# Performance work log

Measured on AMD Instinct MI355X. Metric: run time of the kernel, lower is better.

Reference implementation:

```python
import jax, jax.numpy as jnp
import numpy as np
import math

B, T, C = 4, 2048, 2048
NUM_HEADS = 16
HEAD_DIM = C // NUM_HEADS  # 128
ROPE_BASE = 10000.0


def _rope_tables(t, head_dim, dtype):
    # inv_freq over even dims; emb = concat(freqs, freqs)
    inv_freq = 1.0 / (ROPE_BASE ** (jnp.arange(0, head_dim, 2, dtype=jnp.float32) / head_dim))
    pos = jnp.arange(t, dtype=jnp.float32)
    freqs = jnp.einsum('i,j->ij', pos, inv_freq)          # [t, head_dim/2]
    emb = jnp.concatenate([freqs, freqs], axis=-1)        # [t, head_dim]
    return jnp.cos(emb).astype(dtype), jnp.sin(emb).astype(dtype)


def _rotate_half(x):
    x1, x2 = jnp.split(x, 2, axis=-1)
    return jnp.concatenate([-x2, x1], axis=-1)


def setup_inputs() -> dict:
    key = jax.random.key(0)
    ks = jax.random.split(key, 5)
    scale = 1.0 / math.sqrt(C)
    x = jax.random.normal(ks[0], (B, T, C), dtype=jnp.float32)
    wq = jax.random.normal(ks[1], (C, C), dtype=jnp.float32) * scale
    wk = jax.random.normal(ks[2], (C, C), dtype=jnp.float32) * scale
    wv = jax.random.normal(ks[3], (C, C), dtype=jnp.float32) * scale
    wo = jax.random.normal(ks[4], (C, C), dtype=jnp.float32) * scale
    mask = jnp.tril(jnp.ones((T, T), dtype=jnp.int32))[None, None]  # causal [1,1,T,T]
    return {"x": x, "mask": mask, "wq": wq, "wk": wk, "wv": wv, "wo": wo}


def reference(x, mask, wq, wk, wv, wo):
    b, t, c = x.shape
    h, hd = NUM_HEADS, HEAD_DIM
    # torch Linear: y = x @ W.T (W is [out,in])
    q = (x @ wq.T).reshape(b, t, h, hd).transpose(0, 2, 1, 3)  # [b,h,t,hd]
    k = (x @ wk.T).reshape(b, t, h, hd).transpose(0, 2, 1, 3)
    v = (x @ wv.T).reshape(b, t, h, hd).transpose(0, 2, 1, 3)
    cos, sin = _rope_tables(t, hd, x.dtype)  # [t,hd] each, broadcast over b,h
    q = q * cos + _rotate_half(q) * sin
    k = k * cos + _rotate_half(k) * sin
    att = jnp.einsum('bhqd,bhkd->bhqk', q, k) * (1.0 / math.sqrt(hd))
    att = jnp.where(mask == 0, -jnp.inf, att)
    att = jax.nn.softmax(att, axis=-1)
    y = jnp.einsum('bhqk,bhkd->bhqd', att, v)
    y = y.transpose(0, 2, 1, 3).reshape(b, t, c)
    return y @ wo.T
```

## Files before the change

### kernel.cpp

```cpp
#include <hip/hip_runtime.h>
#include <hip/hip_bf16.h>

#define BB 4
#define TT 2048
#define CC 2048
#define NH 16
#define HD 128
#define BT (BB*TT)

using u16 = unsigned short;
typedef __bf16 bf16x8 __attribute__((ext_vector_type(8)));
typedef float  f32x4  __attribute__((ext_vector_type(4)));

#define AS1 __attribute__((address_space(1)))
#define AS3 __attribute__((address_space(3)))

__device__ __forceinline__ float b2f(u16 u){ return __uint_as_float(((unsigned)u) << 16); }
__device__ __forceinline__ u16 f2b(float f){
  unsigned u = __float_as_uint(f);
  u += 0x7FFFu + ((u >> 16) & 1u);
  return (u16)(u >> 16);
}
__device__ __forceinline__ void gld_lds16(const u16* g, u16* l){
  __builtin_amdgcn_global_load_lds((const AS1 void*)g, (AS3 void*)l, 16, 0, 0);
}

__global__ __launch_bounds__(256) void cvt_kernel(const float* __restrict__ in,
                                                  u16* __restrict__ out, int n8)
{
  const int i = blockIdx.x * 256 + threadIdx.x;
  if (i >= n8) return;
  const float4 a = ((const float4*)in)[2*i];
  const float4 b = ((const float4*)in)[2*i + 1];
  uint4 pk;
  pk.x = (unsigned)f2b(a.x) | ((unsigned)f2b(a.y) << 16);
  pk.y = (unsigned)f2b(a.z) | ((unsigned)f2b(a.w) << 16);
  pk.z = (unsigned)f2b(b.x) | ((unsigned)f2b(b.y) << 16);
  pk.w = (unsigned)f2b(b.z) | ((unsigned)f2b(b.w) << 16);
  ((uint4*)out)[i] = pk;
}

template<bool OUT_BF16>
__global__ __launch_bounds__(512, 2) void gemm256(const u16* __restrict__ A,
                                                  const u16* __restrict__ W,
                                                  void* __restrict__ Cv,
                                                  int K, int N,
                                                  long wz, long cz)
{
  __shared__ u16 lds[65536];
  const int tid  = threadIdx.x;
  const int lane = tid & 63;
  const int wid  = tid >> 6;
  const int wm   = wid >> 2;
  const int wn   = wid & 3;

  const u16* Wz = W + (size_t)blockIdx.z * wz;

  const int nwg  = (int)(gridDim.x * gridDim.y);
  const int orig = (int)(blockIdx.y * gridDim.x + blockIdx.x);
  const int swz  = (orig & 7) * (nwg >> 3) + (orig >> 3);
  const int bx   = swz % (int)gridDim.x;
  const int by   = swz / (int)gridDim.x;
  const long mbase = (long)by * 256;
  const long nbase = (long)bx * 256;

  const int sR  = tid >> 2;
  const int sG8 = (((tid & 3) ^ (sR & 3)) << 3);
  const u16* gA = A  + (mbase + sR) * (long)K + sG8;
  const u16* gB = Wz + (nbase + sR) * (long)K + sG8;
  const long rowK = (long)128 * K;

  const int n   = lane & 15;
  const int g   = lane >> 4;
  const int sl8 = ((g ^ (n & 3)) << 3);
  const int aoff = (wm*128 + n)*32 + sl8;
  const int boff = 8192 + (wn*64 + n)*32 + sl8;

  f32x4 acc[8][4] = {};
  const int NT = K >> 5;

#define STAGE_A(bufi, tt) do { \
    u16* d_ = lds + (bufi)*16384 + tid*8; \
    gld_lds16(gA + (long)(tt)*32,        d_); \
    gld_lds16(gA + rowK + (long)(tt)*32, d_ + 4096); } while(0)
#define STAGE_B(bufi, tt) do { \
    u16* d_ = lds + (bufi)*16384 + 8192 + tid*8; \
    gld_lds16(gB + (long)(tt)*32,        d_); \
    gld_lds16(gB + rowK + (long)(tt)*32, d_ + 4096); } while(0)

  STAGE_A(0, 0); STAGE_B(0, 0);
  STAGE_A(1, 1); STAGE_B(1, 1);
  STAGE_A(2, 2); STAGE_B(2, 2);
  asm volatile("s_waitcnt vmcnt(4)" ::: "memory");
  __builtin_amdgcn_s_barrier();
  asm volatile("" ::: "memory");

  bf16x8 pa0A[4], pb0A[4], a1A[4], pa0B[4], pb0B[4], a1B[4];
  #pragma unroll
  for (int i = 0; i < 4; i++) pa0A[i] = *(const bf16x8*)&lds[aoff + i*512];
  #pragma unroll
  for (int j = 0; j < 4; j++) pb0A[j] = *(const bf16x8*)&lds[boff + j*512];

  for (int t = 0; t < NT; t += 2) {
    {
      const u16* Ab = lds + (t & 3) * 16384;
      const u16* Nb = lds + ((t+1) & 3) * 16384;
      if (t + 3 < NT) STAGE_A((t+3)&3, t+3);
      #pragma unroll
      for (int i = 0; i < 4; i++) a1A[i]  = *(const bf16x8*)&Ab[aoff + (i+4)*512];
      #pragma unroll
      for (int i = 0; i < 4; i++) pa0B[i] = *(const bf16x8*)&Nb[aoff + i*512];
      #pragma unroll
      for (int j = 0; j < 4; j++) pb0B[j] = *(const bf16x8*)&Nb[boff + j*512];
      if (t + 3 < NT) STAGE_B((t+3)&3, t+3);
      __builtin_amdgcn_s_setprio(1);
      #pragma unroll
      for (int i = 0; i < 4; i++)
        #pragma unroll
        for (int j = 0; j < 4; j++)
          acc[i][j] = __builtin_amdgcn_mfma_f32_16x16x32_bf16(pa0A[i], pb0A[j], acc[i][j], 0,0,0);
      #pragma unroll
      for (int i = 0; i < 4; i++)
        #pragma unroll
        for (int j = 0; j < 4; j++)
          acc[i+4][j] = __builtin_amdgcn_mfma_f32_16x16x32_bf16(a1A[i], pb0A[j], acc[i+4][j], 0,0,0);
      __builtin_amdgcn_s_setprio(0);
      if (t + 3 < NT) { asm volatile("s_waitcnt vmcnt(4)" ::: "memory"); }
      else            { asm volatile("s_waitcnt vmcnt(0)" ::: "memory"); }
      __builtin_amdgcn_s_barrier();
      asm volatile("" ::: "memory");
    }
    {
      const int u = t + 1;
      const u16* Ab = lds + (u & 3) * 16384;
      if (u + 3 < NT) STAGE_A((u+3)&3, u+3);
      #pragma unroll
      for (int i = 0; i < 4; i++) a1B[i] = *(const bf16x8*)&Ab[aoff + (i+4)*512];
      if (u + 1 < NT) {
        const u16* Nb = lds + ((u+1) & 3) * 16384;
        #pragma unroll
        for (int i = 0; i < 4; i++) pa0A[i] = *(const bf16x8*)&Nb[aoff + i*512];
        #pragma unroll
        for (int j = 0; j < 4; j++) pb0A[j] = *(const bf16x8*)&Nb[boff + j*512];
      }
      if (u + 3 < NT) STAGE_B((u+3)&3, u+3);
      __builtin_amdgcn_s_setprio(1);
      #pragma unroll
      for (int i = 0; i < 4; i++)
        #pragma unroll
        for (int j = 0; j < 4; j++)
          acc[i][j] = __builtin_amdgcn_mfma_f32_16x16x32_bf16(pa0B[i], pb0B[j], acc[i][j], 0,0,0);
      #pragma unroll
      for (int i = 0; i < 4; i++)
        #pragma unroll
        for (int j = 0; j < 4; j++)
          acc[i+4][j] = __builtin_amdgcn_mfma_f32_16x16x32_bf16(a1B[i], pb0B[j], acc[i+4][j], 0,0,0);
      __builtin_amdgcn_s_setprio(0);
      if (u + 3 < NT) { asm volatile("s_waitcnt vmcnt(4)" ::: "memory"); }
      else            { asm volatile("s_waitcnt vmcnt(0)" ::: "memory"); }
      __builtin_amdgcn_s_barrier();
      asm volatile("" ::: "memory");
    }
  }
#undef STAGE_A
#undef STAGE_B

  const int crow0 = g * 4;
  u16*   C16 = (u16*)Cv   + (size_t)blockIdx.z * cz;
  float* C32 = (float*)Cv;
  #pragma unroll
  for (int i = 0; i < 8; i++)
    #pragma unroll
    for (int j = 0; j < 4; j++)
      #pragma unroll
      for (int r = 0; r < 4; r++) {
        const long row = mbase + wm*128 + i*16 + crow0 + r;
        const long col = nbase + wn*64  + j*16 + n;
        if (OUT_BF16) C16[row*N + col] = f2b(acc[i][j][r]);
        else          C32[row*N + col] = acc[i][j][r];
      }
}

__global__ __launch_bounds__(256) void rope_kernel(u16* __restrict__ q, u16* __restrict__ k)
{
  const unsigned idx = blockIdx.x * 256u + threadIdx.x;
  const int d = idx & 63;
  const int h = (idx >> 6) & 15;
  const int t = (idx >> 10) & 2047;
  const int b = idx >> 21;
  const float inv = __expf(-9.210340371976184f * ((float)d * (1.0f/64.0f)));
  const float ang = (float)t * inv;
  float sn, cs;
  sincosf(ang, &sn, &cs);
  const size_t base = ((size_t)(b * TT + t)) * CC + (size_t)h * HD + d;
  const float q0 = b2f(q[base]), q1 = b2f(q[base + 64]);
  q[base]      = f2b(q0*cs - q1*sn);
  q[base + 64] = f2b(q1*cs + q0*sn);
  const float k0 = b2f(k[base]), k1 = b2f(k[base + 64]);
  k[base]      = f2b(k0*cs - k1*sn);
  k[base + 64] = f2b(k1*cs + k0*sn);
}

__global__ __launch_bounds__(256) void transpose_v(const u16* __restrict__ v,
                                                   u16* __restrict__ vt)
{
  __shared__ u16 L[64][136];
  const int tid = threadIdx.x;
  const int t0 = blockIdx.x * 64;
  const int b = blockIdx.y >> 4, h = blockIdx.y & 15;
  #pragma unroll
  for (int it = 0; it < 4; it++) {
    const int row = (tid >> 4) + it*16;
    const int c8 = (tid & 15) * 8;
    *(uint4*)&L[row][c8] = *(const uint4*)(v + ((size_t)(b*TT + t0 + row))*CC + h*HD + c8);
  }
  __syncthreads();
  #pragma unroll
  for (int it = 0; it < 4; it++) {
    const int hd = (tid >> 3) + it*32;
    const int c = (tid & 7) * 8;
    u16 tmp[8];
    #pragma unroll
    for (int j = 0; j < 8; j++) tmp[j] = L[c + j][hd];
    uint4 pk;
    pk.x = (unsigned)tmp[0] | ((unsigned)tmp[1] << 16);
    pk.y = (unsigned)tmp[2] | ((unsigned)tmp[3] << 16);
    pk.z = (unsigned)tmp[4] | ((unsigned)tmp[5] << 16);
    pk.w = (unsigned)tmp[6] | ((unsigned)tmp[7] << 16);
    *(uint4*)(vt + ((size_t)((b*NH + h)*HD + hd))*TT + t0 + c) = pk;
  }
}

#define PS_ST 72
#define OB_ST 136
__global__ __launch_bounds__(256, 2) void attn_mfma(const u16* __restrict__ q,
                                                    const u16* __restrict__ k,
                                                    const u16* __restrict__ vt,
                                                    u16* __restrict__ y)
{
  __shared__ u16 smem[2*64*128 + 128*64 + 4*32*PS_ST];
  u16* Ks = smem;
  u16* Vs = smem + 16384;
  u16* Ps = smem + 16384 + 8192;

  const int tid  = threadIdx.x;
  const int lane = tid & 63;
  const int w    = tid >> 6;
  const int n    = lane & 15;
  const int g    = lane >> 4;
  const int k8   = g * 8;
  const int nx   = n & 7;
  const int qb   = (int)gridDim.x - 1 - (int)blockIdx.x;
  const int bh   = blockIdx.y;
  const int b = bh >> 4, h = bh & 15;

  const u16* Qg  = q  + (size_t)b*TT*CC + (size_t)h*HD;
  const u16* Kg  = k  + (size_t)b*TT*CC + (size_t)h*HD;
  const u16* Vtg = vt + ((size_t)(b*NH + h)*HD) * TT;
  u16*       Yg  = y  + (size_t)b*TT*CC + (size_t)h*HD;

  const int ksrow = tid >> 4;
  const int kgc   = ((tid & 15) ^ (ksrow & 7)) * 8;
  const int vsrow = tid >> 3;
  const int vgc   = ((tid & 7) ^ (vsrow & 7)) * 8;
  const u16* KgS = Kg  + (size_t)ksrow*CC + kgc;
  const u16* VgS = Vtg + (size_t)vsrow*TT + vgc;

  bf16x8 qf[2][4];
  #pragma unroll
  for (int mi = 0; mi < 2; mi++)
    #pragma unroll
    for (int s = 0; s < 4; s++)
      qf[mi][s] = *(const bf16x8*)(Qg + (size_t)(qb*128 + w*32 + mi*16 + n)*CC + s*32 + k8);

  f32x4 o[8][2] = {};
  float lrow[2][4] = {};

  u16* Psw = Ps + w * 32 * PS_ST;
  const float scale = 0.08838834764831845f;
  const int ktmax = 2*qb + 1;

  {
    u16* dk = Ks + tid*8;
    #pragma unroll
    for (int it = 0; it < 4; it++)
      gld_lds16(KgS + (size_t)(it*16)*CC, dk + it*2048);
  }
  __syncthreads();

  for (int kt = 0; kt <= ktmax; kt++) {
    const int p = kt & 1;
    {
      u16* dv = Vs + tid*8;
      #pragma unroll
      for (int it = 0; it < 4; it++)
        gld_lds16(VgS + (size_t)(it*32)*TT + kt*64, dv + it*2048);
    }
    if (kt < ktmax) {
      u16* dk = Ks + (p^1)*8192 + tid*8;
      #pragma unroll
      for (int it = 0; it < 4; it++)
        gld_lds16(KgS + (size_t)((kt+1)*64 + it*16)*CC, dk + it*2048);
    }

    const u16* Kb = Ks + p*8192;
    f32x4 sacc[4][2] = {};
    __builtin_amdgcn_s_setprio(1);
    #pragma unroll
    for (int s = 0; s < 4; s++) {
      #pragma unroll
      for (int j = 0; j < 4; j++) {
        const bf16x8 kb = *(const bf16x8*)&Kb[(16*j + n)*128 + (((s*4 + g) ^ nx) << 3)];
        sacc[j][0] = __builtin_amdgcn_mfma_f32_16x16x32_bf16(qf[0][s], kb, sacc[j][0], 0,0,0);
        sacc[j][1] = __builtin_amdgcn_mfma_f32_16x16x32_bf16(qf[1][s], kb, sacc[j][1], 0,0,0);
      }
    }
    __builtin_amdgcn_s_setprio(0);

    if (kt >= 2*qb) {
      #pragma unroll
      for (int mi = 0; mi < 2; mi++)
        #pragma unroll
        for (int j = 0; j < 4; j++)
          #pragma unroll
          for (int r = 0; r < 4; r++) {
            const int kcol = kt*64 + 16*j + n;
            const int qrow = qb*128 + w*32 + mi*16 + 4*g + r;
            if (kcol > qrow) sacc[j][mi][r] = -1e30f;
          }
    }

    #pragma unroll
    for (int mi = 0; mi < 2; mi++)
      #pragma unroll
      for (int j = 0; j < 4; j++)
        #pragma unroll
        for (int r = 0; r < 4; r++) {
          const float pv = __expf(sacc[j][mi][r] * scale);
          lrow[mi][r] += pv;
          Psw[(mi*16 + 4*g + r)*PS_ST + 16*j + n] = f2b(pv);
        }

    if (kt < ktmax) { asm volatile("s_waitcnt vmcnt(4) lgkmcnt(0)" ::: "memory"); }
    else            { asm volatile("s_waitcnt vmcnt(0) lgkmcnt(0)" ::: "memory"); }
    __builtin_amdgcn_s_barrier();
    asm volatile("" ::: "memory");

    __builtin_amdgcn_s_setprio(1);
    #pragma unroll
    for (int s2 = 0; s2 < 2; s2++) {
      const bf16x8 pa0 = *(const bf16x8*)&Psw[(n)*PS_ST      + s2*32 + k8];
      const bf16x8 pa1 = *(const bf16x8*)&Psw[(16 + n)*PS_ST + s2*32 + k8];
      #pragma unroll
      for (int jo = 0; jo < 8; jo++) {
        const bf16x8 vb = *(const bf16x8*)&Vs[(16*jo + n)*64 + (((s2*4 + g) ^ nx) << 3)];
        o[jo][0] = __builtin_amdgcn_mfma_f32_16x16x32_bf16(pa0, vb, o[jo][0], 0,0,0);
        o[jo][1] = __builtin_amdgcn_mfma_f32_16x16x32_bf16(pa1, vb, o[jo][1], 0,0,0);
      }
    }
    __builtin_amdgcn_s_setprio(0);

    __syncthreads();
  }

  #pragma unroll
  for (int mi = 0; mi < 2; mi++)
    #pragma unroll
    for (int r = 0; r < 4; r++) {
      float sv = lrow[mi][r];
      #pragma unroll
      for (int msk = 1; msk <= 8; msk <<= 1) sv += __shfl_xor(sv, msk);
      lrow[mi][r] = sv;
    }

  u16* Ob = smem;
  #pragma unroll
  for (int mi = 0; mi < 2; mi++) {
    float inv[4];
    #pragma unroll
    for (int r = 0; r < 4; r++) inv[r] = 1.0f / lrow[mi][r];
    #pragma unroll
    for (int jo = 0; jo < 8; jo++)
      #pragma unroll
      for (int r = 0; r < 4; r++)
        Ob[(w*32 + mi*16 + 4*g + r)*OB_ST + 16*jo + n] = f2b(o[jo][mi][r] * inv[r]);
  }
  __syncthreads();
  #pragma unroll
  for (int it = 0; it < 8; it++) {
    const int idx = it*64 + lane;
    const int row = idx >> 4;
    const int ch  = (idx & 15) * 8;
    const uint4 pk = *(const uint4*)&Ob[(w*32 + row)*OB_ST + ch];
    *(uint4*)(Yg + (size_t)(qb*128 + w*32 + row)*CC + ch) = pk;
  }
}

extern "C" void kernel_launch(void* const* d_in, const int* in_sizes, int n_in,
                              void* d_out, int out_size, void* d_ws, size_t ws_size,
                              hipStream_t stream)
{
  const float* x  = (const float*)d_in[0];
  const float* wq = (const float*)d_in[2];
  const float* wk = (const float*)d_in[3];
  const float* wv = (const float*)d_in[4];
  const float* wo = (const float*)d_in[5];

  const size_t NE  = (size_t)BT * CC;
  const size_t NW  = (size_t)CC * CC;
  u16* q  = (u16*)d_ws;
  u16* k  = q  + NE;
  u16* v  = k  + NE;
  u16* y  = v  + NE;
  u16* xb = y  + NE;
  u16* wqb = xb + NE;
  u16* wkb = wqb + NW;
  u16* wvb = wkb + NW;
  u16* wob = wvb + NW;
  u16* vt  = xb;

  cvt_kernel<<<(int)(NE/8/256), 256, 0, stream>>>(x,  xb,  (int)(NE/8));
  cvt_kernel<<<(int)(NW/8/256), 256, 0, stream>>>(wq, wqb, (int)(NW/8));
  cvt_kernel<<<(int)(NW/8/256), 256, 0, stream>>>(wk, wkb, (int)(NW/8));
  cvt_kernel<<<(int)(NW/8/256), 256, 0, stream>>>(wv, wvb, (int)(NW/8));
  cvt_kernel<<<(int)(NW/8/256), 256, 0, stream>>>(wo, wob, (int)(NW/8));

  gemm256<true><<<dim3(8, 32, 3), 512, 0, stream>>>(xb, wqb, q, CC, CC,
                                                    (long)NW, (long)NE);

  rope_kernel<<<(BB*TT*NH*64)/256, 256, 0, stream>>>(q, k);

  transpose_v<<<dim3(TT/64, BB*NH), 256, 0, stream>>>(v, vt);

  attn_mfma<<<dim3(TT/128, BB*NH), 256, 0, stream>>>(q, k, vt, y);

  gemm256<false><<<dim3(8, 32, 1), 512, 0, stream>>>(y, wob, (float*)d_out, CC, CC,
                                                     0L, 0L);
}
```

Baseline: 618.3 us.

## Keep attention P in registers via transposed QK MFMA and double-buffer V

The QK^T MFMA operands are swapped so each lane holds scores for one query row. P is then packed to bf16 with v_cvt_pk_bf16_f32 and rearranged through cross-lane shuffles into the A-operand layout of the PV MFMA, which removes the LDS round-trip for P and the mid-iteration barrier. V tiles are now double-buffered and prefetched one iteration ahead alongside K, and the GEMM LDS swizzle pattern is changed. The cost is extra shuffle instructions and a larger LDS footprint for V, which may affect occupancy.

```diff
diff --git a/kernel.cpp b/kernel.cpp
--- a/kernel.cpp
+++ b/kernel.cpp
@@ -65,14 +65,14 @@
   const long nbase = (long)bx * 256;
 
   const int sR  = tid >> 2;
-  const int sG8 = (((tid & 3) ^ (sR & 3)) << 3);
+  const int sG8 = (((tid & 3) ^ ((sR >> 1) & 3)) << 3);
   const u16* gA = A  + (mbase + sR) * (long)K + sG8;
   const u16* gB = Wz + (nbase + sR) * (long)K + sG8;
   const long rowK = (long)128 * K;
 
   const int n   = lane & 15;
   const int g   = lane >> 4;
-  const int sl8 = ((g ^ (n & 3)) << 3);
+  const int sl8 = ((g ^ ((n >> 1) & 3)) << 3);
   const int aoff = (wm*128 + n)*32 + sl8;
   const int boff = 8192 + (wn*64 + n)*32 + sl8;
 
@@ -231,17 +231,15 @@
   }
 }
 
-#define PS_ST 72
 #define OB_ST 136
 __global__ __launch_bounds__(256, 2) void attn_mfma(const u16* __restrict__ q,
                                                     const u16* __restrict__ k,
                                                     const u16* __restrict__ vt,
                                                     u16* __restrict__ y)
 {
-  __shared__ u16 smem[2*64*128 + 128*64 + 4*32*PS_ST];
+  __shared__ u16 smem[4*64*128];
   u16* Ks = smem;
   u16* Vs = smem + 16384;
-  u16* Ps = smem + 16384 + 8192;
 
   const int tid  = threadIdx.x;
   const int lane = tid & 63;
@@ -274,9 +272,8 @@
       qf[mi][s] = *(const bf16x8*)(Qg + (size_t)(qb*128 + w*32 + mi*16 + n)*CC + s*32 + k8);
 
   f32x4 o[8][2] = {};
-  float lrow[2][4] = {};
-
-  u16* Psw = Ps + w * 32 * PS_ST;
+  float lrow[2] = {};
+
   const float scale = 0.08838834764831845f;
   const int ktmax = 2*qb + 1;
 
@@ -285,22 +282,24 @@
     #pragma unroll
     for (int it = 0; it < 4; it++)
       gld_lds16(KgS + (size_t)(it*16)*CC, dk + it*2048);
+    u16* dv = Vs + tid*8;
+    #pragma unroll
+    for (int it = 0; it < 4; it++)
+      gld_lds16(VgS + (size_t)(it*32)*TT, dv + it*2048);
   }
   __syncthreads();
 
   for (int kt = 0; kt <= ktmax; kt++) {
     const int p = kt & 1;
-    {
-      u16* dv = Vs + tid*8;
-      #pragma unroll
-      for (int it = 0; it < 4; it++)
-        gld_lds16(VgS + (size_t)(it*32)*TT + kt*64, dv + it*2048);
-    }
     if (kt < ktmax) {
       u16* dk = Ks + (p^1)*8192 + tid*8;
       #pragma unroll
       for (int it = 0; it < 4; it++)
         gld_lds16(KgS + (size_t)((kt+1)*64 + it*16)*CC, dk + it*2048);
+      u16* dv = Vs + (p^1)*8192 + tid*8;
+      #pragma unroll
+      for (int it = 0; it < 4; it++)
+        gld_lds16(VgS + (size_t)(it*32)*TT + (kt+1)*64, dv + it*2048);
     }
 
     const u16* Kb = Ks + p*8192;
@@ -311,8 +310,8 @@
       #pragma unroll
       for (int j = 0; j < 4; j++) {
         const bf16x8 kb = *(const bf16x8*)&Kb[(16*j + n)*128 + (((s*4 + g) ^ nx) << 3)];
-        sacc[j][0] = __builtin_amdgcn_mfma_f32_16x16x32_bf16(qf[0][s], kb, sacc[j][0], 0,0,0);
-        sacc[j][1] = __builtin_amdgcn_mfma_f32_16x16x32_bf16(qf[1][s], kb, sacc[j][1], 0,0,0);
+        sacc[j][0] = __builtin_amdgcn_mfma_f32_16x16x32_bf16(kb, qf[0][s], sacc[j][0], 0,0,0);
+        sacc[j][1] = __builtin_amdgcn_mfma_f32_16x16x32_bf16(kb, qf[1][s], sacc[j][1], 0,0,0);
       }
     }
     __builtin_amdgcn_s_setprio(0);
@@ -324,36 +323,52 @@
         for (int j = 0; j < 4; j++)
           #pragma unroll
           for (int r = 0; r < 4; r++) {
-            const int kcol = kt*64 + 16*j + n;
-            const int qrow = qb*128 + w*32 + mi*16 + 4*g + r;
+            const int kcol = kt*64 + 16*j + 4*g + r;
+            const int qrow = qb*128 + w*32 + mi*16 + n;
             if (kcol > qrow) sacc[j][mi][r] = -1e30f;
           }
     }
 
+    unsigned P2[4][2][2];
+    #pragma unroll
+    for (int j = 0; j < 4; j++)
+      #pragma unroll
+      for (int mi = 0; mi < 2; mi++) {
+        const float e0 = __expf(sacc[j][mi][0] * scale);
+        const float e1 = __expf(sacc[j][mi][1] * scale);
+        const float e2 = __expf(sacc[j][mi][2] * scale);
+        const float e3 = __expf(sacc[j][mi][3] * scale);
+        lrow[mi] += (e0 + e1) + (e2 + e3);
+        asm("v_cvt_pk_bf16_f32 %0, %1, %2" : "=v"(P2[j][mi][0]) : "v"(e0), "v"(e1));
+        asm("v_cvt_pk_bf16_f32 %0, %1, %2" : "=v"(P2[j][mi][1]) : "v"(e2), "v"(e3));
+      }
+
+    uint4 pa[2][2];
     #pragma unroll
     for (int mi = 0; mi < 2; mi++)
       #pragma unroll
-      for (int j = 0; j < 4; j++)
-        #pragma unroll
-        for (int r = 0; r < 4; r++) {
-          const float pv = __expf(sacc[j][mi][r] * scale);
-          lrow[mi][r] += pv;
-          Psw[(mi*16 + 4*g + r)*PS_ST + 16*j + n] = f2b(pv);
+      for (int s2 = 0; s2 < 2; s2++) {
+        unsigned wv[4];
+        #pragma unroll
+        for (int ww = 0; ww < 4; ww++) {
+          const int src = n + 16*((2*g + (ww>>1)) & 3);
+          const unsigned lo = __shfl(P2[2*s2    ][mi][ww & 1], src);
+          const unsigned hi = __shfl(P2[2*s2 + 1][mi][ww & 1], src);
+          wv[ww] = (g & 2) ? hi : lo;
         }
-
-    if (kt < ktmax) { asm volatile("s_waitcnt vmcnt(4) lgkmcnt(0)" ::: "memory"); }
-    else            { asm volatile("s_waitcnt vmcnt(0) lgkmcnt(0)" ::: "memory"); }
-    __builtin_amdgcn_s_barrier();
-    asm volatile("" ::: "memory");
-
+        pa[mi][s2].x = wv[0]; pa[mi][s2].y = wv[1];
+        pa[mi][s2].z = wv[2]; pa[mi][s2].w = wv[3];
+      }
+
+    const u16* Vb = Vs + p*8192;
     __builtin_amdgcn_s_setprio(1);
     #pragma unroll
     for (int s2 = 0; s2 < 2; s2++) {
-      const bf16x8 pa0 = *(const bf16x8*)&Psw[(n)*PS_ST      + s2*32 + k8];
-      const bf16x8 pa1 = *(const bf16x8*)&Psw[(16 + n)*PS_ST + s2*32 + k8];
+      const bf16x8 pa0 = *(const bf16x8*)&pa[0][s2];
+      const bf16x8 pa1 = *(const bf16x8*)&pa[1][s2];
       #pragma unroll
       for (int jo = 0; jo < 8; jo++) {
-        const bf16x8 vb = *(const bf16x8*)&Vs[(16*jo + n)*64 + (((s2*4 + g) ^ nx) << 3)];
+        const bf16x8 vb = *(const bf16x8*)&Vb[(16*jo + n)*64 + (((s2*4 + g) ^ nx) << 3)];
         o[jo][0] = __builtin_amdgcn_mfma_f32_16x16x32_bf16(pa0, vb, o[jo][0], 0,0,0);
         o[jo][1] = __builtin_amdgcn_mfma_f32_16x16x32_bf16(pa1, vb, o[jo][1], 0,0,0);
       }
@@ -364,21 +379,19 @@
   }
 
   #pragma unroll
-  for (int mi = 0; mi < 2; mi++)
-    #pragma unroll
-    for (int r = 0; r < 4; r++) {
-      float sv = lrow[mi][r];
-      #pragma unroll
-      for (int msk = 1; msk <= 8; msk <<= 1) sv += __shfl_xor(sv, msk);
-      lrow[mi][r] = sv;
-    }
+  for (int mi = 0; mi < 2; mi++) {
+    float sv = lrow[mi];
+    sv += __shfl_xor(sv, 16);
+    sv += __shfl_xor(sv, 32);
+    lrow[mi] = sv;
+  }
 
   u16* Ob = smem;
   #pragma unroll
   for (int mi = 0; mi < 2; mi++) {
     float inv[4];
     #pragma unroll
-    for (int r = 0; r < 4; r++) inv[r] = 1.0f / lrow[mi][r];
+    for (int r = 0; r < 4; r++) inv[r] = 1.0f / __shfl(lrow[mi], 4*g + r);
     #pragma unroll
     for (int jo = 0; jo < 8; jo++)
       #pragma unroll
```

Result: no change. 610.8 us (-1.2%).
